# Performance work log

Hardware: AMD Instinct MI355X
Metric: run time of the kernel (lower is better)

## Reference

```python
import jax, jax.numpy as jnp
import numpy as np

INPUT_DIM = 100
LATENT_DIM = 128
HIDDEN_DIM = 64
BATCH = 16384


def setup_inputs() -> dict:
    key = jax.random.key(0)
    ku, k1, kb1, k2, kb2 = jax.random.split(key, 5)
    u = jax.random.normal(ku, (BATCH, INPUT_DIM), dtype=jnp.float32)
    # PyTorch Linear init: U(-1/sqrt(fan_in), 1/sqrt(fan_in))
    s1 = 1.0 / np.sqrt(INPUT_DIM)
    s2 = 1.0 / np.sqrt(HIDDEN_DIM)
    W1 = jax.random.uniform(k1, (LATENT_DIM, HIDDEN_DIM, INPUT_DIM), jnp.float32, -s1, s1)
    b1 = jax.random.uniform(kb1, (LATENT_DIM, HIDDEN_DIM), jnp.float32, -s1, s1)
    W2 = jax.random.uniform(k2, (LATENT_DIM, HIDDEN_DIM), jnp.float32, -s2, s2)  # out_features=1 squeezed
    b2 = jax.random.uniform(kb2, (LATENT_DIM,), jnp.float32, -s2, s2)
    return {"u": u, "W1": W1, "b1": b1, "W2": W2, "b2": b2}


def reference(u, W1, b1, W2, b2):
    # All latent_dim branches batched as one grouped GEMM.
    # h: [batch, latent, hidden]
    h = jnp.tanh(jnp.einsum('bi,khi->bkh', u, W1) + b1[None, :, :])
    # out: [batch, latent]  (second Linear has output dim 1, squeezed)
    out = jnp.einsum('bkh,kh->bk', h, W2) + b2[None, :]
    return out
```

## Files before the change

### kernel.cpp

```cpp
#include <hip/hip_runtime.h>

#define BATCH 16384
#define LATENT 128
#define HIDDEN 64
#define INDIM 100
#define KPAD 128
#define TANH_SCALE 2.885390081777927f

typedef short shortx8 __attribute__((ext_vector_type(8)));
typedef float floatx4 __attribute__((ext_vector_type(4)));

__device__ __forceinline__ unsigned bfbits(float f) {
    union { float f; unsigned u; } v; v.f = f;
    return (v.u + 0x7FFF + ((v.u >> 16) & 1)) >> 16;
}

#if __has_builtin(__builtin_amdgcn_exp2f)
#define EXP2F(x) __builtin_amdgcn_exp2f(x)
#else
#define EXP2F(x) __exp2f(x)
#endif
#if __has_builtin(__builtin_amdgcn_rcpf)
#define RCPF(x) __builtin_amdgcn_rcpf(x)
#else
#define RCPF(x) (1.0f / (x))
#endif

#define N_U_BLK (BATCH / 16)
#define N_W_BLK (LATENT * HIDDEN / 16)

__global__ __launch_bounds__(256) void prep_all(const float* __restrict__ u,
                                                const float* __restrict__ W1,
                                                const float* __restrict__ b1,
                                                const float* __restrict__ W2,
                                                const float* __restrict__ b2,
                                                shortx8* __restrict__ uf,
                                                shortx8* __restrict__ wf,
                                                float* __restrict__ b2eff) {
    int bx = blockIdx.x;
    int tid = threadIdx.x;

    if (bx >= N_U_BLK + N_W_BLK) {
        if (tid < LATENT) {
            float s = b2[tid];
            const float* wp = W2 + tid * HIDDEN;
#pragma unroll 8
            for (int h = 0; h < HIDDEN; h++) s += wp[h];
            b2eff[tid] = s;
        }
        return;
    }

    bool isW = (bx >= N_U_BLK);
    int tileIdx = isW ? (bx - N_U_BLK) : bx;
    int r0 = tileIdx * 16;
    const float* src = isW ? W1 : u;
    float scale = isW ? TANH_SCALE : 1.0f;

    __shared__ short lds[16 * 136];

#pragma unroll
    for (int it = 0; it < 4; it++) {
        int p = it * 256 + tid;
        int rl = p >> 6;
        int kp = (p & 63) * 2;
        float f0 = 0.0f, f1 = 0.0f;
        if (kp < INDIM) {
            const float2 t = *(const float2*)(src + (r0 + rl) * INDIM + kp);
            f0 = t.x * scale; f1 = t.y * scale;
        } else if (kp == INDIM) {
            f0 = isW ? b1[r0 + rl] * TANH_SCALE : 1.0f;
        }
        *(unsigned*)(&lds[rl * 136 + kp]) = bfbits(f0) | (bfbits(f1) << 16);
    }
    __syncthreads();

    {
        int lane = tid & 63;
        int kt = tid >> 6;
        int rl = lane & 15;
        int kb = kt * 32 + ((lane >> 4) << 3);
        shortx8 v = *(const shortx8*)(&lds[rl * 136 + kb]);
        shortx8* dst = isW ? wf : uf;
        dst[((size_t)tileIdx * 4 + kt) * 64 + lane] = v;
    }
}

__global__ __launch_bounds__(256, 4) void branch_mlp(const shortx8* __restrict__ uf,
                                                     const shortx8* __restrict__ wf,
                                                     const float* __restrict__ W2,
                                                     const float* __restrict__ b2eff,
                                                     float* __restrict__ out) {
    int tid = threadIdx.x;
    int lane = tid & 63;
    int w = tid >> 6;
    int bx = blockIdx.x;
    int lat = bx >> 5;
    int G0 = (bx & 31) * 32 + w * 8;
    int q = lane >> 4;

    shortx8 afr[4][4];
    const shortx8* wb = wf + (size_t)lat * 16 * 64 + lane;
#pragma unroll
    for (int nt = 0; nt < 4; nt++)
#pragma unroll
        for (int kt = 0; kt < 4; kt++)
            afr[nt][kt] = wb[(nt * 4 + kt) * 64];

    float4 w2v[4];
#pragma unroll
    for (int nt = 0; nt < 4; nt++) {
        float4 t = *(const float4*)(W2 + lat * HIDDEN + nt * 16 + q * 4);
        w2v[nt] = make_float4(-2.0f * t.x, -2.0f * t.y, -2.0f * t.z, -2.0f * t.w);
    }
    float b2v = b2eff[lat];

    const shortx8* ua = uf + (size_t)G0 * 4 * 64 + lane;

    float sg[8];
#pragma unroll
    for (int g = 0; g < 8; g++) {
        shortx8 ub[4];
#pragma unroll
        for (int kt = 0; kt < 4; kt++)
            ub[kt] = ua[(g * 4 + kt) * 64];

        floatx4 acc[4] = {};
#pragma unroll
        for (int kt = 0; kt < 4; kt++)
#pragma unroll
            for (int nt = 0; nt < 4; nt++)
                acc[nt] = __builtin_amdgcn_mfma_f32_16x16x32_bf16(afr[nt][kt], ub[kt], acc[nt], 0, 0, 0);

        float s = 0.0f;
#pragma unroll
        for (int nt = 0; nt < 4; nt++)
#pragma unroll
            for (int r = 0; r < 4; r++) {
                float e = EXP2F(acc[nt][r]);
                float rr = RCPF(e + 1.0f);
                s = fmaf((&w2v[nt].x)[r], rr, s);
            }
        sg[g] = s;
    }

#pragma unroll
    for (int g = 0; g < 8; g++) sg[g] += __shfl_xor(sg[g], 16, 64);
#pragma unroll
    for (int g = 0; g < 8; g++) sg[g] += __shfl_xor(sg[g], 32, 64);
    if (lane < 16) {
        float* outp = out + ((size_t)G0 * 16 + lane) * LATENT + lat;
#pragma unroll
        for (int g = 0; g < 8; g++)
            outp[g * 16 * LATENT] = sg[g] + b2v;
    }
}

__global__ __launch_bounds__(256) void fallback_kernel(const float* __restrict__ u, const float* __restrict__ W1,
                                                       const float* __restrict__ b1, const float* __restrict__ W2,
                                                       const float* __restrict__ b2, float* __restrict__ out) {
    int idx = blockIdx.x * 256 + threadIdx.x;
    if (idx >= BATCH * LATENT) return;
    int b = idx >> 7;
    int lat = idx & 127;
    const float* ub = u + b * INDIM;
    float s = 0.0f;
    for (int h = 0; h < HIDDEN; h++) {
        const float* wp = W1 + (lat * HIDDEN + h) * INDIM;
        float dd = b1[lat * HIDDEN + h];
        for (int k = 0; k < INDIM; k++) dd += ub[k] * wp[k];
        s += tanhf(dd) * W2[lat * HIDDEN + h];
    }
    out[idx] = s + b2[lat];
}

extern "C" void kernel_launch(void* const* d_in, const int* in_sizes, int n_in,
                              void* d_out, int out_size, void* d_ws, size_t ws_size,
                              hipStream_t stream) {
    const float* u  = (const float*)d_in[0];
    const float* W1 = (const float*)d_in[1];
    const float* b1 = (const float*)d_in[2];
    const float* W2 = (const float*)d_in[3];
    const float* b2 = (const float*)d_in[4];
    float* out = (float*)d_out;

    const size_t UF_BYTES = (size_t)BATCH * KPAD * 2;
    const size_t WF_BYTES = (size_t)LATENT * HIDDEN * KPAD * 2;
    const size_t B2_BYTES = LATENT * sizeof(float);

    if (ws_size < UF_BYTES + WF_BYTES + B2_BYTES) {
        fallback_kernel<<<(BATCH * LATENT + 255) / 256, 256, 0, stream>>>(u, W1, b1, W2, b2, out);
        return;
    }

    shortx8* uf = (shortx8*)d_ws;
    shortx8* wf = (shortx8*)((char*)d_ws + UF_BYTES);
    float* b2eff = (float*)((char*)d_ws + UF_BYTES + WF_BYTES);

    prep_all<<<N_U_BLK + N_W_BLK + 1, 256, 0, stream>>>(u, W1, b1, W2, b2, uf, wf, b2eff);
    branch_mlp<<<4096, 256, 0, stream>>>(uf, wf, W2, b2eff, out);
}
```

Baseline: 114.0 us.

## Stage weight fragments in LDS, pair batch groups, batch reciprocals across four outputs

Each wave no longer keeps the 16 W1 fragments in registers. The block stages them once in LDS and every wave reads them per MFMA. Two batch groups are processed together for more MFMA instruction-level parallelism, and launch bounds drop from 4 to 3 waves per SIMD. The sigmoid-style tanh epilogue replaces four reciprocals with one, by taking the reciprocal of the product of four denominators and multiplying back. This cuts transcendental work but can overflow to zero when pre-activations are large.

```diff
diff --git a/kernel.cpp b/kernel.cpp
--- a/kernel.cpp
+++ b/kernel.cpp
@@ -86,11 +86,12 @@
     }
 }
 
-__global__ __launch_bounds__(256, 4) void branch_mlp(const shortx8* __restrict__ uf,
+__global__ __launch_bounds__(256, 3) void branch_mlp(const shortx8* __restrict__ uf,
                                                      const shortx8* __restrict__ wf,
                                                      const float* __restrict__ W2,
                                                      const float* __restrict__ b2eff,
                                                      float* __restrict__ out) {
+    __shared__ shortx8 wlds[16 * 64];
     int tid = threadIdx.x;
     int lane = tid & 63;
     int w = tid >> 6;
@@ -99,13 +100,14 @@
     int G0 = (bx & 31) * 32 + w * 8;
     int q = lane >> 4;
 
-    shortx8 afr[4][4];
-    const shortx8* wb = wf + (size_t)lat * 16 * 64 + lane;
-#pragma unroll
-    for (int nt = 0; nt < 4; nt++)
-#pragma unroll
-        for (int kt = 0; kt < 4; kt++)
-            afr[nt][kt] = wb[(nt * 4 + kt) * 64];
+    {
+        const shortx8* wfl = wf + (size_t)lat * 16 * 64;
+#pragma unroll
+        for (int j = 0; j < 4; j++) {
+            int i = j * 256 + tid;
+            wlds[i] = wfl[i];
+        }
+    }
 
     float4 w2v[4];
 #pragma unroll
@@ -115,33 +117,51 @@
     }
     float b2v = b2eff[lat];
 
+    __syncthreads();
+
     const shortx8* ua = uf + (size_t)G0 * 4 * 64 + lane;
 
     float sg[8];
 #pragma unroll
-    for (int g = 0; g < 8; g++) {
-        shortx8 ub[4];
+    for (int p = 0; p < 4; p++) {
+        shortx8 ub0[4], ub1[4];
+#pragma unroll
+        for (int kt = 0; kt < 4; kt++) {
+            ub0[kt] = ua[((2 * p) * 4 + kt) * 64];
+            ub1[kt] = ua[((2 * p + 1) * 4 + kt) * 64];
+        }
+
+        floatx4 acc0[4] = {}, acc1[4] = {};
 #pragma unroll
         for (int kt = 0; kt < 4; kt++)
-            ub[kt] = ua[(g * 4 + kt) * 64];
-
-        floatx4 acc[4] = {};
-#pragma unroll
-        for (int kt = 0; kt < 4; kt++)
-#pragma unroll
-            for (int nt = 0; nt < 4; nt++)
-                acc[nt] = __builtin_amdgcn_mfma_f32_16x16x32_bf16(afr[nt][kt], ub[kt], acc[nt], 0, 0, 0);
-
-        float s = 0.0f;
-#pragma unroll
-        for (int nt = 0; nt < 4; nt++)
-#pragma unroll
-            for (int r = 0; r < 4; r++) {
-                float e = EXP2F(acc[nt][r]);
-                float rr = RCPF(e + 1.0f);
-                s = fmaf((&w2v[nt].x)[r], rr, s);
+#pragma unroll
+            for (int nt = 0; nt < 4; nt++) {
+                shortx8 afr = wlds[(nt * 4 + kt) * 64 + lane];
+                acc0[nt] = __builtin_amdgcn_mfma_f32_16x16x32_bf16(afr, ub0[kt], acc0[nt], 0, 0, 0);
+                acc1[nt] = __builtin_amdgcn_mfma_f32_16x16x32_bf16(afr, ub1[kt], acc1[nt], 0, 0, 0);
             }
-        sg[g] = s;
+
+#pragma unroll
+        for (int e = 0; e < 2; e++) {
+            const floatx4* ac = e ? acc1 : acc0;
+            float s = 0.0f;
+#pragma unroll
+            for (int nt = 0; nt < 4; nt++) {
+                float d0 = EXP2F(ac[nt][0]) + 1.0f;
+                float d1 = EXP2F(ac[nt][1]) + 1.0f;
+                float d2 = EXP2F(ac[nt][2]) + 1.0f;
+                float d3 = EXP2F(ac[nt][3]) + 1.0f;
+                float p01 = d0 * d1, p23 = d2 * d3;
+                float ip = RCPF(p01 * p23);
+                float r01 = ip * p23;
+                float r23 = ip * p01;
+                s = fmaf(w2v[nt].x, r01 * d1, s);
+                s = fmaf(w2v[nt].y, r01 * d0, s);
+                s = fmaf(w2v[nt].z, r23 * d3, s);
+                s = fmaf(w2v[nt].w, r23 * d2, s);
+            }
+            sg[2 * p + e] = s;
+        }
     }
 
 #pragma unroll
```

After: 116.4 us. 1.02x slower.
